# Kernel tuning notes

Hardware: AMD Instinct MI355X
Metric: run time of the kernel (lower is better)

The kernel has to match this reference:

```python
import jax, jax.numpy as jnp
import numpy as np

N = 50000
E = 800000
IN_C, HID_C, OUT_C = 512, 128, 64


def setup_inputs() -> dict:
    key = jax.random.key(0)
    k = jax.random.split(key, 8)
    x = jax.random.normal(k[0], (N, IN_C), dtype=jnp.float32)
    edge_index = jax.random.randint(k[1], (2, E), 0, N, dtype=jnp.int64)
    edge_weight = jax.random.uniform(k[2], (E,), dtype=jnp.float32)
    # GCNConv parameters (glorot-like init)
    W1 = jax.random.normal(k[3], (IN_C, HID_C), dtype=jnp.float32) * (1.0 / np.sqrt(IN_C))
    b1 = jnp.zeros((HID_C,), dtype=jnp.float32)
    W2 = jax.random.normal(k[4], (HID_C, OUT_C), dtype=jnp.float32) * (1.0 / np.sqrt(HID_C))
    b2 = jnp.zeros((OUT_C,), dtype=jnp.float32)
    return {"x": x, "edge_index": edge_index, "edge_weight": edge_weight,
            "W1": W1, "b1": b1, "W2": W2, "b2": b2}


def _add_self_loops(edge_index, edge_weight, num_nodes):
    loop = jnp.arange(num_nodes, dtype=edge_index.dtype)
    ei = jnp.concatenate([edge_index, jnp.stack([loop, loop])], axis=1)
    ew = jnp.concatenate([edge_weight, jnp.ones((num_nodes,), edge_weight.dtype)])
    return ei, ew


def _gcn_conv(x, row, col, norm, W, b, num_nodes):
    # linear transform first (PyG GCNConv), then normalized scatter-add aggregation
    xw = x @ W                                    # [N, F_out]
    msg = norm[:, None] * xw[row]                 # gather + scale, [E', F_out]
    out = jnp.zeros((num_nodes, xw.shape[1]), xw.dtype).at[col].add(msg)
    return out + b


def reference(x, edge_index, edge_weight, W1, b1, W2, b2):
    num_nodes = x.shape[0]
    ei, ew = _add_self_loops(edge_index, edge_weight, num_nodes)
    row, col = ei[0], ei[1]
    # symmetric normalization: D^{-1/2} A D^{-1/2} (deg over destination index)
    deg = jnp.zeros((num_nodes,), ew.dtype).at[col].add(ew)
    dinv = jnp.where(deg > 0, jax.lax.rsqrt(deg), 0.0)
    norm = dinv[row] * ew * dinv[col]
    h = _gcn_conv(x, row, col, norm, W1, b1, num_nodes)
    h = jax.nn.relu(h)
    # dropout p=0.5 is identity in eval mode
    return _gcn_conv(h, row, col, norm, W2, b2, num_nodes)
```

## Files before the change

### kernel.cpp

```cpp
#include <hip/hip_runtime.h>

#define NNODES 50000
#define NEDGES 800000
#define IN_C   512
#define HID_C  128
#define OUT_C  64
#define NBUCK  196
#define BCAP   5120
#define BREG   5376

typedef float  f32x4  __attribute__((ext_vector_type(4)));
typedef __bf16 bf16x8 __attribute__((ext_vector_type(8)));
typedef short  short8 __attribute__((ext_vector_type(8)));

#define GLDS(src, dst) \
  __builtin_amdgcn_global_load_lds( \
      (const __attribute__((address_space(1))) unsigned int*)(src), \
      (__attribute__((address_space(3))) unsigned int*)(dst), 16, 0, 0)

__device__ __forceinline__ float bf2f(unsigned short u) {
  unsigned int x = (unsigned int)u << 16;
  return __builtin_bit_cast(float, x);
}
__device__ __forceinline__ unsigned short f16bits(float f) {
  _Float16 h = (_Float16)f;
  return __builtin_bit_cast(unsigned short, h);
}
__device__ __forceinline__ float f16val(unsigned short u) {
  return (float)__builtin_bit_cast(_Float16, u);
}


__device__ __forceinline__ void wsplit_one(const float* __restrict__ W,
                                           unsigned short* __restrict__ Th,
                                           unsigned short* __restrict__ Tl,
                                           int K, int N, int id) {
  int k = id % K, n = id / K;
  float f = W[(size_t)k * N + n];
  __bf16 hb = (__bf16)f;
  __bf16 lb = (__bf16)(f - (float)hb);
  Th[id] = __builtin_bit_cast(unsigned short, hb);
  Tl[id] = __builtin_bit_cast(unsigned short, lb);
}

__global__ void __launch_bounds__(256) prep0_kernel(
    unsigned int* __restrict__ gclaim,
    const float* __restrict__ W1, unsigned short* __restrict__ W1th,
    unsigned short* __restrict__ W1tl,
    const float* __restrict__ W2, unsigned short* __restrict__ W2th,
    unsigned short* __restrict__ W2tl) {
  int id = blockIdx.x * blockDim.x + threadIdx.x;
  if (id < 256) { if (id < NBUCK) gclaim[id] = (unsigned int)id * BCAP; return; }
  int s = id - 256;
  if (s < IN_C * HID_C) wsplit_one(W1, W1th, W1tl, IN_C, HID_C, s);
  else if (s < IN_C * HID_C + HID_C * OUT_C)
    wsplit_one(W2, W2th, W2tl, HID_C, OUT_C, s - IN_C * HID_C);
}

template <int K, int N, int WR, int WC>
__device__ __forceinline__ void gemm_body(const float* __restrict__ X,
                                          const unsigned short* __restrict__ Bth,
                                          const unsigned short* __restrict__ Btl,
                                          unsigned short* __restrict__ Y, int M, int bid) {
  constexpr int NW = WR * WC;
  constexpr int BM = WR * 32;
  constexpr int NI = K / 32;
  constexpr int ASLOTS = (BM / 8) / NW;
  constexpr int BSLOTS = (N / 8) / NW;

  __shared__ float          As[2][BM * 32];
  __shared__ unsigned short Bs[2][2][N * 32];

  int tid = threadIdx.x;
  int lane = tid & 63, wid = tid >> 6;
  int wr = wid / WC, wc = wid % WC;
  int row0blk = bid * BM;
  int row0 = row0blk + wr * 32;
  int rlo = lane & 15;
  int khi = lane >> 4;

  f32x4 acc[2][4] = {};

  auto stage = [&](int t, int buf) {
    int kb = t * 32;
#pragma unroll
    for (int i = 0; i < ASLOTS; ++i) {
      int slot = wid * ASLOTS + i;
      int rt = slot * 8 + (lane >> 3);
      int gr = row0blk + rt; gr = gr < M ? gr : M - 1;
      int gs = (lane & 7) ^ (lane >> 3);
      GLDS(X + (size_t)gr * K + kb + gs * 4, &As[buf][slot * 256]);
    }
#pragma unroll
    for (int i = 0; i < BSLOTS; ++i) {
      int slot = wid * BSLOTS + i;
      int half = slot / (N / 16);
      int idx = slot % (N / 16);
      const unsigned short* Wt = half ? Btl : Bth;
      int c = idx * 16 + (lane >> 2);
      int gs = (lane & 3) ^ (lane >> 4);
      GLDS(Wt + (size_t)c * K + kb + gs * 8, &Bs[buf][half][idx * 512]);
    }
  };

  stage(0, 0);
  __syncthreads();

#pragma unroll 1
  for (int t = 0; t < NI; ++t) {
    int buf = t & 1;
    if (t + 1 < NI) stage(t + 1, buf ^ 1);

    bf16x8 ah[2], al[2];
#pragma unroll
    for (int m = 0; m < 2; ++m) {
      int rt = wr * 32 + m * 16 + rlo;
      int p0 = (khi * 2) ^ (rlo & 7), p1 = (khi * 2 + 1) ^ (rlo & 7);
      f32x4 v0 = *reinterpret_cast<const f32x4*>(&As[buf][rt * 32 + p0 * 4]);
      f32x4 v1 = *reinterpret_cast<const f32x4*>(&As[buf][rt * 32 + p1 * 4]);
      float f[8] = {v0.x, v0.y, v0.z, v0.w, v1.x, v1.y, v1.z, v1.w};
#pragma unroll
      for (int i = 0; i < 8; ++i) {
        __bf16 hv = (__bf16)f[i];
        ah[m][i] = hv;
        al[m][i] = (__bf16)(f[i] - (float)hv);
      }
    }
    short8 bh[4], bl[4];
#pragma unroll
    for (int n = 0; n < 4; ++n) {
      int c = wc * 64 + n * 16 + rlo;
      int pos = khi ^ (rlo >> 2);
      bh[n] = *reinterpret_cast<const short8*>(&Bs[buf][0][c * 32 + pos * 8]);
      bl[n] = *reinterpret_cast<const short8*>(&Bs[buf][1][c * 32 + pos * 8]);
    }
#pragma unroll
    for (int m = 0; m < 2; ++m)
#pragma unroll
      for (int n = 0; n < 4; ++n)
        acc[m][n] = __builtin_amdgcn_mfma_f32_16x16x32_bf16(
            ah[m], __builtin_bit_cast(bf16x8, bh[n]), acc[m][n], 0, 0, 0);
#pragma unroll
    for (int m = 0; m < 2; ++m)
#pragma unroll
      for (int n = 0; n < 4; ++n)
        acc[m][n] = __builtin_amdgcn_mfma_f32_16x16x32_bf16(
            al[m], __builtin_bit_cast(bf16x8, bh[n]), acc[m][n], 0, 0, 0);
#pragma unroll
    for (int m = 0; m < 2; ++m)
#pragma unroll
      for (int n = 0; n < 4; ++n)
        acc[m][n] = __builtin_amdgcn_mfma_f32_16x16x32_bf16(
            ah[m], __builtin_bit_cast(bf16x8, bl[n]), acc[m][n], 0, 0, 0);
    __syncthreads();
  }

#pragma unroll
  for (int m = 0; m < 2; ++m)
#pragma unroll
    for (int j = 0; j < 4; ++j) {
      int row = row0 + m * 16 + khi * 4 + j;
      if (row < M) {
#pragma unroll
        for (int n = 0; n < 4; ++n) {
          __bf16 q = (__bf16)acc[m][n][j];
          Y[(size_t)row * N + wc * 64 + n * 16 + rlo] = __builtin_bit_cast(unsigned short, q);
        }
      }
    }
}

__global__ void __launch_bounds__(512, 4) fused_gemm1_scatter_kernel(
    const float* __restrict__ X, const unsigned short* __restrict__ Bth,
    const unsigned short* __restrict__ Btl, unsigned short* __restrict__ Y, int M,
    int ngemm, const int* __restrict__ ei, const float* __restrict__ ew,
    unsigned int* __restrict__ gclaim, unsigned long long* __restrict__ binned, int nE) {
  if ((int)blockIdx.x < ngemm) {
    gemm_body<IN_C, HID_C, 4, 2>(X, Bth, Btl, Y, M, blockIdx.x);
    return;
  }
  __shared__ unsigned int h[NBUCK];
  __shared__ unsigned int cur[NBUCK];
  int t = threadIdx.x;
  if (t < NBUCK) h[t] = 0;
  __syncthreads();
  int base = ((int)blockIdx.x - ngemm) * 4096;
  int r[8]; unsigned int c[8]; unsigned short wb[8];
#pragma unroll
  for (int i = 0; i < 8; ++i) {
    int e = base + i * 512 + t;
    if (e < nE) {
      r[i] = ei[e];
      c[i] = (unsigned int)ei[nE + e];
      wb[i] = f16bits(ew[e]);
      atomicAdd(&h[c[i] >> 8], 1u);
    } else {
      c[i] = 0xFFFFFFFFu;
    }
  }
  __syncthreads();
  if (t < NBUCK) cur[t] = h[t] ? atomicAdd(&gclaim[t], h[t]) : 0u;
  __syncthreads();
#pragma unroll
  for (int i = 0; i < 8; ++i) {
    if (c[i] != 0xFFFFFFFFu) {
      unsigned int pos = atomicAdd(&cur[c[i] >> 8], 1u);
      unsigned long long rec = (unsigned long long)((unsigned int)r[i] & 0xFFFFu)
                             | ((unsigned long long)(c[i] & 0xFFu) << 16)
                             | ((unsigned long long)wb[i] << 32);
      binned[pos] = rec;
    }
  }
}


__global__ void __launch_bounds__(256) bucket_build_kernel(
    const unsigned long long* __restrict__ binned, const unsigned int* __restrict__ gclaim,
    float* __restrict__ dinv, int* __restrict__ offs, unsigned short* __restrict__ cnts,
    unsigned int* __restrict__ edges) {
  int b = blockIdx.x, t = threadIdx.x;
  int base = b * BCAP;
  int cnt = (int)gclaim[b] - base;
  int nb = min(256, NNODES - b * 256);
  int csrbase = b * BREG;
  __shared__ unsigned int ec[256], wf[256], cur[256];
  __shared__ int sc[256];
  __shared__ unsigned int image[BREG];
  ec[t] = 0; wf[t] = 0;
  __syncthreads();
  for (int i = t; i < cnt; i += 256) {
    unsigned long long rec = binned[base + i];
    int dlo = (int)((rec >> 16) & 255ULL);
    atomicAdd(&ec[dlo], 1u);
    float w = f16val((unsigned short)(rec >> 32));
    atomicAdd(&wf[dlo], (unsigned int)(w * 1048576.0f + 0.5f));
  }
  __syncthreads();
  int cn = (t < nb) ? (int)ec[t] + 1 : 0;
  sc[t] = cn;
  __syncthreads();
  for (int off = 1; off < 256; off <<= 1) {
    int u = (t >= off) ? sc[t - off] : 0;
    __syncthreads();
    sc[t] += u;
    __syncthreads();
  }
  if (t < nb) {
    float deg = (float)wf[t] * (1.0f / 1048576.0f) + 1.0f;
    int g = b * 256 + t;
    float di = rsqrtf(deg);
    dinv[g] = di;
    int loc = sc[t] - cn;
    offs[g] = csrbase + loc;
    cnts[g] = (unsigned short)ec[t];
    cur[t] = (unsigned int)(loc + 1);
    image[loc] = (unsigned int)g | (0x3C00u << 16);
  }
  __syncthreads();
  for (int i = t; i < cnt; i += 256) {
    unsigned long long rec = binned[base + i];
    int src = (int)(rec & 0xFFFFULL);
    int dlo = (int)((rec >> 16) & 255ULL);
    unsigned int wb = (unsigned int)((rec >> 32) & 0xFFFFULL);
    unsigned int pos = atomicAdd(&cur[dlo], 1u);
    image[pos] = (unsigned int)src | (wb << 16);
  }
  __syncthreads();
  int total = cnt + nb;
  for (int j = t; j < total; j += 256) edges[csrbase + j] = image[j];
}

template <int K, int N, int WR, int WC>
__global__ void __launch_bounds__(WR * WC * 64, 4) gemm_bf16a_kernel(
    const unsigned short* __restrict__ X, const unsigned short* __restrict__ Bth,
    const unsigned short* __restrict__ Btl, unsigned short* __restrict__ Y, int M) {
  constexpr int NW = WR * WC;
  constexpr int BM = WR * 32;
  constexpr int NI = K / 32;
  constexpr int ASLOTS = (BM / 16) / NW;
  constexpr int BSLOTS = (N / 8) / NW;

  __shared__ unsigned short As[2][BM * 32];
  __shared__ unsigned short Bs[2][2][N * 32];

  int tid = threadIdx.x;
  int lane = tid & 63, wid = tid >> 6;
  int wr = wid / WC, wc = wid % WC;
  int row0blk = blockIdx.x * BM;
  int row0 = row0blk + wr * 32;
  int rlo = lane & 15;
  int khi = lane >> 4;

  f32x4 acc[2][4] = {};

  auto stage = [&](int t, int buf) {
    int kb = t * 32;
#pragma unroll
    for (int i = 0; i < ASLOTS; ++i) {
      int slot = wid * ASLOTS + i;
      int rt = slot * 16 + (lane >> 2);
      int gr = row0blk + rt; gr = gr < M ? gr : M - 1;
      int gs = (lane & 3) ^ ((lane >> 3) & 3);
      GLDS(X + (size_t)gr * K + kb + gs * 8, &As[buf][slot * 512]);
    }
#pragma unroll
    for (int i = 0; i < BSLOTS; ++i) {
      int slot = wid * BSLOTS + i;
      int half = slot / (N / 16);
      int idx = slot % (N / 16);
      const unsigned short* Wt = half ? Btl : Bth;
      int c = idx * 16 + (lane >> 2);
      int gs = (lane & 3) ^ (lane >> 4);
      GLDS(Wt + (size_t)c * K + kb + gs * 8, &Bs[buf][half][idx * 512]);
    }
  };

  stage(0, 0);
  __syncthreads();

#pragma unroll 1
  for (int t = 0; t < NI; ++t) {
    int buf = t & 1;
    if (t + 1 < NI) stage(t + 1, buf ^ 1);

    short8 ah[2];
#pragma unroll
    for (int m = 0; m < 2; ++m) {
      int rt = wr * 32 + m * 16 + rlo;
      int g = khi ^ ((rt >> 1) & 3);
      ah[m] = *reinterpret_cast<const short8*>(&As[buf][rt * 32 + g * 8]);
    }
    short8 bh[4], bl[4];
#pragma unroll
    for (int n = 0; n < 4; ++n) {
      int c = wc * 64 + n * 16 + rlo;
      int pos = khi ^ (rlo >> 2);
      bh[n] = *reinterpret_cast<const short8*>(&Bs[buf][0][c * 32 + pos * 8]);
      bl[n] = *reinterpret_cast<const short8*>(&Bs[buf][1][c * 32 + pos * 8]);
    }
#pragma unroll
    for (int m = 0; m < 2; ++m)
#pragma unroll
      for (int n = 0; n < 4; ++n)
        acc[m][n] = __builtin_amdgcn_mfma_f32_16x16x32_bf16(
            __builtin_bit_cast(bf16x8, ah[m]), __builtin_bit_cast(bf16x8, bh[n]),
            acc[m][n], 0, 0, 0);
#pragma unroll
    for (int m = 0; m < 2; ++m)
#pragma unroll
      for (int n = 0; n < 4; ++n)
        acc[m][n] = __builtin_amdgcn_mfma_f32_16x16x32_bf16(
            __builtin_bit_cast(bf16x8, ah[m]), __builtin_bit_cast(bf16x8, bl[n]),
            acc[m][n], 0, 0, 0);
    __syncthreads();
  }

#pragma unroll
  for (int m = 0; m < 2; ++m)
#pragma unroll
    for (int j = 0; j < 4; ++j) {
      int row = row0 + m * 16 + khi * 4 + j;
      if (row < M) {
#pragma unroll
        for (int n = 0; n < 4; ++n) {
          __bf16 q = (__bf16)acc[m][n][j];
          Y[(size_t)row * N + wc * 64 + n * 16 + rlo] = __builtin_bit_cast(unsigned short, q);
        }
      }
    }
}

template <int F, bool RELU, bool OUTBF>
__global__ void __launch_bounds__(256) agg_kernel(const unsigned short* __restrict__ feat,
                                                  const int* __restrict__ offs,
                                                  const unsigned short* __restrict__ cnts,
                                                  const unsigned int* __restrict__ edges,
                                                  const float* __restrict__ dinv,
                                                  const float* __restrict__ bias,
                                                  void* __restrict__ outv, int n) {
  constexpr int LPN = F / 8;
  constexpr int NPW = 64 / LPN;
  constexpr int NPB = 4 * NPW;
  int wid = threadIdx.x >> 6;
  int lane = threadIdx.x & 63;
  int node = blockIdx.x * NPB + wid * NPW + lane / LPN;
  int lf = (lane % LPN) * 8;
  if (node >= n) return;
  int e0 = offs[node];
  int e1 = e0 + 1 + (int)cnts[node];

  float acc[8] = {};

  auto fmaEdge = [&](unsigned int q) {
    int row = (int)(q & 0xFFFFu);
    float w = f16val((unsigned short)(q >> 16)) * dinv[row];
    short8 v = *reinterpret_cast<const short8*>(&feat[(size_t)row * F + lf]);
#pragma unroll
    for (int j = 0; j < 8; ++j)
      acc[j] = fmaf(w, bf2f((unsigned short)v[j]), acc[j]);
  };

  int e = e0;
  for (; e + 4 <= e1; e += 4) {
    unsigned int q0 = edges[e], q1 = edges[e + 1], q2 = edges[e + 2], q3 = edges[e + 3];
    fmaEdge(q0); fmaEdge(q1); fmaEdge(q2); fmaEdge(q3);
  }
  for (; e < e1; ++e) fmaEdge(edges[e]);

  float dd = dinv[node];
#pragma unroll
  for (int j = 0; j < 8; ++j) {
    acc[j] = fmaf(acc[j], dd, bias[lf + j]);
    if (RELU) acc[j] = fmaxf(acc[j], 0.f);
  }
  if constexpr (OUTBF) {
    short8 o;
#pragma unroll
    for (int j = 0; j < 8; ++j) {
      __bf16 q = (__bf16)acc[j];
      o[j] = (short)__builtin_bit_cast(unsigned short, q);
    }
    *reinterpret_cast<short8*>((unsigned short*)outv + (size_t)node * F + lf) = o;
  } else {
    float* out = (float*)outv;
    float4 o0 = make_float4(acc[0], acc[1], acc[2], acc[3]);
    float4 o1 = make_float4(acc[4], acc[5], acc[6], acc[7]);
    *reinterpret_cast<float4*>(&out[(size_t)node * F + lf]) = o0;
    *reinterpret_cast<float4*>(&out[(size_t)node * F + lf + 4]) = o1;
  }
}


extern "C" void kernel_launch(void* const* d_in, const int* in_sizes, int n_in,
                              void* d_out, int out_size, void* d_ws, size_t ws_size,
                              hipStream_t stream) {
  const float* x  = (const float*)d_in[0];
  const int*   ei = (const int*)d_in[1];
  const float* ew = (const float*)d_in[2];
  const float* W1 = (const float*)d_in[3];
  const float* b1 = (const float*)d_in[4];
  const float* W2 = (const float*)d_in[5];
  const float* b2 = (const float*)d_in[6];
  float* out = (float*)d_out;

  const int N = NNODES, E = NEDGES;

  char* p = (char*)d_ws;
  auto alloc = [&](size_t bytes) { char* r = p; p += (bytes + 255) & ~(size_t)255; return r; };
  unsigned int* gclaim = (unsigned int*)alloc(256 * 4);
  float* dinv   = (float*)alloc((size_t)N * 4);
  int*   offs   = (int*)  alloc((size_t)N * 4);
  unsigned short* cnts = (unsigned short*)alloc((size_t)N * 2);
  unsigned long long* binned = (unsigned long long*)alloc((size_t)NBUCK * BCAP * 8);
  unsigned int* edges  = (unsigned int*)alloc((size_t)NBUCK * BREG * 4);
  unsigned short* xw = (unsigned short*)alloc((size_t)N * HID_C * 2);
  unsigned short* h  = (unsigned short*)alloc((size_t)N * HID_C * 2);
  unsigned short* W1th = (unsigned short*)alloc((size_t)IN_C * HID_C * 2);
  unsigned short* W1tl = (unsigned short*)alloc((size_t)IN_C * HID_C * 2);
  unsigned short* W2th = (unsigned short*)alloc((size_t)HID_C * OUT_C * 2);
  unsigned short* W2tl = (unsigned short*)alloc((size_t)HID_C * OUT_C * 2);

  const int PREP0 = 256 + IN_C * HID_C + HID_C * OUT_C;
  prep0_kernel<<<(PREP0 + 255) / 256, 256, 0, stream>>>(
      gclaim, W1, W1th, W1tl, W2, W2th, W2tl);

  const int NGEMM = (N + 127) / 128;
  const int NSCAT = (E + 4095) / 4096;
  fused_gemm1_scatter_kernel<<<NGEMM + NSCAT, 512, 0, stream>>>(
      x, W1th, W1tl, xw, N, NGEMM, ei, ew, gclaim, binned, E);

  bucket_build_kernel<<<NBUCK, 256, 0, stream>>>(binned, gclaim, dinv, offs, cnts, edges);

  agg_kernel<HID_C, true, true><<<(N + 15) / 16, 256, 0, stream>>>(
      xw, offs, cnts, edges, dinv, b1, h, N);

  gemm_bf16a_kernel<HID_C, OUT_C, 8, 1><<<(N + 255) / 256, 512, 0, stream>>>(h, W2th, W2tl, xw, N);
  agg_kernel<OUT_C, false, false><<<(N + 31) / 32, 256, 0, stream>>>(
      xw, offs, cnts, edges, dinv, b2, out, N);
}
```

Measured before the change: 106.8 us.

## Deepen GEMM pipelines to four LDS buffers with vmcnt waits and reorder fused blocks

```diff
diff --git a/kernel.cpp b/kernel.cpp
--- a/kernel.cpp
+++ b/kernel.cpp
@@ -28,6 +28,16 @@
 }
 __device__ __forceinline__ float f16val(unsigned short u) {
   return (float)__builtin_bit_cast(_Float16, u);
+}
+
+template <int LPS>
+__device__ __forceinline__ void pipe_wait_barrier(int rem) {
+  __builtin_amdgcn_sched_barrier(0);
+  if (rem >= 2)      asm volatile("s_waitcnt vmcnt(%0)" :: "i"(2 * LPS) : "memory");
+  else if (rem == 1) asm volatile("s_waitcnt vmcnt(%0)" :: "i"(LPS) : "memory");
+  else               asm volatile("s_waitcnt vmcnt(0)" ::: "memory");
+  __builtin_amdgcn_s_barrier();
+  __builtin_amdgcn_sched_barrier(0);
 }
 
 
@@ -67,9 +77,11 @@
   constexpr int NI = K / 32;
   constexpr int ASLOTS = (BM / 8) / NW;
   constexpr int BSLOTS = (N / 8) / NW;
-
-  __shared__ float          As[2][BM * 32];
-  __shared__ unsigned short Bs[2][2][N * 32];
+  constexpr int LPS = ASLOTS + 2 * BSLOTS / 2 + BSLOTS / 2;
+  constexpr int LOADS = ASLOTS + BSLOTS;
+
+  __shared__ float          As[4][BM * 32];
+  __shared__ unsigned short Bs[4][2][N * 32];
 
   int tid = threadIdx.x;
   int lane = tid & 63, wid = tid >> 6;
@@ -103,13 +115,13 @@
     }
   };
 
-  stage(0, 0);
-  __syncthreads();
+  stage(0, 0); stage(1, 1); stage(2, 2);
 
 #pragma unroll 1
   for (int t = 0; t < NI; ++t) {
-    int buf = t & 1;
-    if (t + 1 < NI) stage(t + 1, buf ^ 1);
+    int buf = t & 3;
+    pipe_wait_barrier<LOADS>(NI - 1 - t);
+    if (t + 3 < NI) stage(t + 3, (t + 3) & 3);
 
     bf16x8 ah[2], al[2];
 #pragma unroll
@@ -152,7 +164,6 @@
       for (int n = 0; n < 4; ++n)
         acc[m][n] = __builtin_amdgcn_mfma_f32_16x16x32_bf16(
             ah[m], __builtin_bit_cast(bf16x8, bl[n]), acc[m][n], 0, 0, 0);
-    __syncthreads();
   }
 
 #pragma unroll
@@ -170,13 +181,13 @@
     }
 }
 
-__global__ void __launch_bounds__(512, 4) fused_gemm1_scatter_kernel(
+__global__ void __launch_bounds__(512) fused_scatter_gemm1_kernel(
     const float* __restrict__ X, const unsigned short* __restrict__ Bth,
     const unsigned short* __restrict__ Btl, unsigned short* __restrict__ Y, int M,
-    int ngemm, const int* __restrict__ ei, const float* __restrict__ ew,
+    int nscat, const int* __restrict__ ei, const float* __restrict__ ew,
     unsigned int* __restrict__ gclaim, unsigned long long* __restrict__ binned, int nE) {
-  if ((int)blockIdx.x < ngemm) {
-    gemm_body<IN_C, HID_C, 4, 2>(X, Bth, Btl, Y, M, blockIdx.x);
+  if ((int)blockIdx.x >= nscat) {
+    gemm_body<IN_C, HID_C, 4, 2>(X, Bth, Btl, Y, M, (int)blockIdx.x - nscat);
     return;
   }
   __shared__ unsigned int h[NBUCK];
@@ -184,7 +195,7 @@
   int t = threadIdx.x;
   if (t < NBUCK) h[t] = 0;
   __syncthreads();
-  int base = ((int)blockIdx.x - ngemm) * 4096;
+  int base = (int)blockIdx.x * 4096;
   int r[8]; unsigned int c[8]; unsigned short wb[8];
 #pragma unroll
   for (int i = 0; i < 8; ++i) {
@@ -212,7 +223,6 @@
     }
   }
 }
-
 
 __global__ void __launch_bounds__(256) bucket_build_kernel(
     const unsigned long long* __restrict__ binned, const unsigned int* __restrict__ gclaim,
@@ -271,7 +281,7 @@
 }
 
 template <int K, int N, int WR, int WC>
-__global__ void __launch_bounds__(WR * WC * 64, 4) gemm_bf16a_kernel(
+__global__ void __launch_bounds__(WR * WC * 64) gemm_bf16a_kernel(
     const unsigned short* __restrict__ X, const unsigned short* __restrict__ Bth,
     const unsigned short* __restrict__ Btl, unsigned short* __restrict__ Y, int M) {
   constexpr int NW = WR * WC;
@@ -279,9 +289,10 @@
   constexpr int NI = K / 32;
   constexpr int ASLOTS = (BM / 16) / NW;
   constexpr int BSLOTS = (N / 8) / NW;
-
-  __shared__ unsigned short As[2][BM * 32];
-  __shared__ unsigned short Bs[2][2][N * 32];
+  constexpr int LOADS = ASLOTS + BSLOTS;
+
+  __shared__ unsigned short As[4][BM * 32];
+  __shared__ unsigned short Bs[4][2][N * 32];
 
   int tid = threadIdx.x;
   int lane = tid & 63, wid = tid >> 6;
@@ -315,13 +326,13 @@
     }
   };
 
-  stage(0, 0);
-  __syncthreads();
+  stage(0, 0); stage(1, 1); stage(2, 2);
 
 #pragma unroll 1
   for (int t = 0; t < NI; ++t) {
-    int buf = t & 1;
-    if (t + 1 < NI) stage(t + 1, buf ^ 1);
+    int buf = t & 3;
+    pipe_wait_barrier<LOADS>(NI - 1 - t);
+    if (t + 3 < NI) stage(t + 3, (t + 3) & 3);
 
     short8 ah[2];
 #pragma unroll
@@ -352,7 +363,6 @@
         acc[m][n] = __builtin_amdgcn_mfma_f32_16x16x32_bf16(
             __builtin_bit_cast(bf16x8, ah[m]), __builtin_bit_cast(bf16x8, bl[n]),
             acc[m][n], 0, 0, 0);
-    __syncthreads();
   }
 
 #pragma unroll
@@ -466,8 +476,8 @@
 
   const int NGEMM = (N + 127) / 128;
   const int NSCAT = (E + 4095) / 4096;
-  fused_gemm1_scatter_kernel<<<NGEMM + NSCAT, 512, 0, stream>>>(
-      x, W1th, W1tl, xw, N, NGEMM, ei, ew, gclaim, binned, E);
+  fused_scatter_gemm1_kernel<<<NSCAT + NGEMM, 512, 0, stream>>>(
+      x, W1th, W1tl, xw, N, NSCAT, ei, ew, gclaim, binned, E);
 
   bucket_build_kernel<<<NBUCK, 256, 0, stream>>>(binned, gclaim, dinv, offs, cnts, edges);
 
```

Result: slower. 128.4 us (+20.3%).
